# Optimization experiments

Hardware: AMD Instinct MI355X
Metric: run time of the kernel (lower is better)

The kernel has to match this reference:

```python
import jax, jax.numpy as jnp
import numpy as np

N_NODES = 100000
N_EDGES = 1600000
N_GRAPHS = 128
H = 64          # hidden_channels_gin
L = 3           # num_layers
IN_X = 4
IN_E = 8
G_DIM = H * L   # pooled concat dim = hidden_channels_global
OUT = 1


def _w(k, shape):
    return (jax.random.normal(k, shape, jnp.float32) * 0.1)


def setup_inputs() -> dict:
    key = jax.random.key(0)
    ks = jax.random.split(key, 24)
    inp = {
        'x': jax.random.normal(ks[0], (N_NODES, IN_X), jnp.float32),
        'edge_index': jax.random.randint(ks[1], (2, N_EDGES), 0, N_NODES),
        'batch': jnp.sort(jax.random.randint(ks[2], (N_NODES,), 0, N_GRAPHS)),
        'edge_attr': jax.random.normal(ks[3], (N_EDGES, IN_E), jnp.float32),
        # node embedding MLP (MLPembd: Linear-ReLU-Linear-ReLU-Linear)
        'nW1': _w(ks[4], (IN_X, H)), 'nb1': jnp.zeros((H,), jnp.float32),
        'nW2': _w(ks[5], (H, H)),    'nb2': jnp.zeros((H,), jnp.float32),
        'nW3': _w(ks[6], (H, H)),    'nb3': jnp.zeros((H,), jnp.float32),
        # edge embedding MLP (gin_MLP_layers[0])
        'eW1': _w(ks[7], (IN_E, H)), 'eb1': jnp.zeros((H,), jnp.float32),
        'eW2': _w(ks[8], (H, H)),    'eb2': jnp.zeros((H,), jnp.float32),
        'eW3': _w(ks[9], (H, H)),    'eb3': jnp.zeros((H,), jnp.float32),
        # GINE layers: trainable eps + 2-layer MLP nn per layer (stacked over L)
        'gine_eps': jnp.zeros((L,), jnp.float32),
        'gW1': _w(ks[10], (L, H, H)), 'gb1': jnp.zeros((L, H), jnp.float32),
        'gW2': _w(ks[11], (L, H, H)), 'gb2': jnp.zeros((L, H), jnp.float32),
        # output MLP: Linear - BN(eval) - LeakyReLU - (Dropout eval) - Linear
        'oW1': _w(ks[12], (G_DIM, G_DIM)), 'ob1': jnp.zeros((G_DIM,), jnp.float32),
        'ogamma': jnp.ones((G_DIM,), jnp.float32), 'obeta': jnp.zeros((G_DIM,), jnp.float32),
        'oW2': _w(ks[13], (G_DIM, OUT)), 'ob2': jnp.zeros((OUT,), jnp.float32),
    }
    return inp


def _mlp3(x, W1, b1, W2, b2, W3, b3):
    x = jax.nn.relu(x @ W1 + b1)
    x = jax.nn.relu(x @ W2 + b2)
    return x @ W3 + b3


def _forward(x, edge_index, batch, edge_attr,
             nW1, nb1, nW2, nb2, nW3, nb3,
             eW1, eb1, eW2, eb2, eW3, eb3,
             gine_eps, gW1, gb1, gW2, gb2,
             oW1, ob1, ogamma, obeta, oW2, ob2):
    src, dst = edge_index[0], edge_index[1]
    h = _mlp3(x, nW1, nb1, nW2, nb2, nW3, nb3)                    # [N, H]
    ea = _mlp3(edge_attr, eW1, eb1, eW2, eb2, eW3, eb3)           # [E, H]
    pooled = []
    for l in range(L):  # fixed small layer count
        msg = jax.nn.leaky_relu(h[src] + ea)                      # [E, H] gather + add
        agg = jax.ops.segment_max(msg, dst, num_segments=N_NODES) # max aggregation
        agg = jnp.where(jnp.isfinite(agg), agg, 0.0)              # isolated nodes -> 0
        z = (1.0 + gine_eps[l]) * h + agg
        h = jax.nn.leaky_relu(z @ gW1[l] + gb1[l]) @ gW2[l] + gb2[l]
        pooled.append(jax.ops.segment_max(h, batch, num_segments=N_GRAPHS))
    hp = jnp.concatenate(pooled, axis=1)                          # [G, H*L]
    y = hp @ oW1 + ob1
    y = ogamma * y + obeta            # eval-mode BatchNorm1d (running mean=0, var=1)
    y = jax.nn.leaky_relu(y)          # Dropout inactive at inference
    logits = y @ oW2 + ob2            # [G, 1]
    return logits, jax.nn.sigmoid(logits)


def reference(x, edge_index, batch, edge_attr,
              nW1, nb1, nW2, nb2, nW3, nb3,
              eW1, eb1, eW2, eb2, eW3, eb3,
              gine_eps, gW1, gb1, gW2, gb2,
              oW1, ob1, ogamma, obeta, oW2, ob2):
    return _forward(x, edge_index, batch, edge_attr,
                    nW1, nb1, nW2, nb2, nW3, nb3,
                    eW1, eb1, eW2, eb2, eW3, eb3,
                    gine_eps, gW1, gb1, gW2, gb2,
                    oW1, ob1, ogamma, obeta, oW2, ob2)
```

## Files before the change

kernel.cpp:

```cpp
#include <hip/hip_runtime.h>
#include <hip/hip_bf16.h>

#define LRELU(x) ((x) > 0.0f ? (x) : 0.01f * (x))

typedef __attribute__((ext_vector_type(4))) short bf16x4;
typedef __attribute__((ext_vector_type(4))) float f32x4;

__device__ __forceinline__ unsigned fenc(float f) {
    unsigned u = __float_as_uint(f);
    return (u & 0x80000000u) ? ~u : (u | 0x80000000u);
}
__device__ __forceinline__ float fdec(unsigned u) {
    return (u & 0x80000000u) ? __uint_as_float(u & 0x7fffffffu) : __uint_as_float(~u);
}
__device__ __forceinline__ short f2bf(float f) {
    __hip_bfloat16 b = __float2bfloat16(f);
    return *reinterpret_cast<short*>(&b);
}
__device__ __forceinline__ float bf2f(short s) {
    return __uint_as_float(((unsigned)(unsigned short)s) << 16);
}

__device__ __forceinline__ f32x4 mfma16(bf16x4 a, bf16x4 b, f32x4 c) {
#if __has_builtin(__builtin_amdgcn_mfma_f32_16x16x16bf16_1k)
    return __builtin_amdgcn_mfma_f32_16x16x16bf16_1k(a, b, c, 0, 0, 0);
#else
    asm("v_mfma_f32_16x16x16_bf16 %0, %1, %2, %0" : "+v"(c) : "v"(a), "v"(b));
    return c;
#endif
}

__global__ __launch_bounds__(256) void hist_kernel(const int* __restrict__ ei,
                                                   int* __restrict__ deg_p,
                                                   int* __restrict__ rank, int E)
{
    const int stride = gridDim.x * blockDim.x * 4;
    const bool vec = ((E & 3) == 0);
    for (int e4 = (blockIdx.x * blockDim.x + threadIdx.x) * 4; e4 < E; e4 += stride) {
        if (vec && e4 + 3 < E) {
            const int4 d = *reinterpret_cast<const int4*>(ei + E + e4);
            int4 r;
            r.x = atomicAdd(&deg_p[(size_t)d.x * 4], 1);
            r.y = atomicAdd(&deg_p[(size_t)d.y * 4], 1);
            r.z = atomicAdd(&deg_p[(size_t)d.z * 4], 1);
            r.w = atomicAdd(&deg_p[(size_t)d.w * 4], 1);
            *reinterpret_cast<int4*>(rank + e4) = r;
        } else {
            for (int k = 0; k < 4 && e4 + k < E; ++k) {
                const int d = ei[E + e4 + k];
                rank[e4 + k] = atomicAdd(&deg_p[(size_t)d * 4], 1);
            }
        }
    }
}

__global__ __launch_bounds__(1024) void scan_kernel(const int* __restrict__ deg_p,
                                                    int* __restrict__ rowptr, int N)
{
    __shared__ int wsum[16];
    __shared__ int tiletot;
    const int lane = threadIdx.x & 63;
    const int w    = threadIdx.x >> 6;
    int carry = 0;
    for (int base = 0; base < N; base += 4096) {
        const int i = base + (int)threadIdx.x * 4;
        int4 v = {0, 0, 0, 0};
        if (i < N)     v.x = deg_p[(size_t)i * 4];
        if (i + 1 < N) v.y = deg_p[(size_t)(i + 1) * 4];
        if (i + 2 < N) v.z = deg_p[(size_t)(i + 2) * 4];
        if (i + 3 < N) v.w = deg_p[(size_t)(i + 3) * 4];
        const int tot = v.x + v.y + v.z + v.w;
        int s = tot;
#pragma unroll
        for (int off = 1; off < 64; off <<= 1) {
            int t = __shfl_up(s, off);
            if (lane >= off) s += t;
        }
        if (lane == 63) wsum[w] = s;
        __syncthreads();
        if (threadIdx.x == 0) {
            int acc = 0;
#pragma unroll
            for (int k = 0; k < 16; ++k) { int t = wsum[k]; wsum[k] = acc; acc += t; }
            tiletot = acc;
        }
        __syncthreads();
        const int excl = carry + wsum[w] + (s - tot);
        int4 o;
        o.x = excl; o.y = excl + v.x; o.z = o.y + v.y; o.w = o.z + v.z;
        if (i + 3 < N) {
            *reinterpret_cast<int4*>(rowptr + i) = o;
        } else {
            if (i < N)     rowptr[i] = o.x;
            if (i + 1 < N) rowptr[i + 1] = o.y;
            if (i + 2 < N) rowptr[i + 2] = o.z;
        }
        carry += tiletot;
        __syncthreads();
    }
    if (threadIdx.x == 0) rowptr[N] = carry;
}

__global__ __launch_bounds__(256) void scatter_kernel(
    const int* __restrict__ ei, const int* __restrict__ rank,
    const int* __restrict__ rowptr, int2* __restrict__ pack, int E)
{
    const int stride = gridDim.x * blockDim.x * 4;
    const bool vec = ((E & 3) == 0);
    for (int e4 = (blockIdx.x * blockDim.x + threadIdx.x) * 4; e4 < E; e4 += stride) {
        if (vec && e4 + 3 < E) {
            const int4 s  = *reinterpret_cast<const int4*>(ei + e4);
            const int4 d  = *reinterpret_cast<const int4*>(ei + E + e4);
            const int4 rk = *reinterpret_cast<const int4*>(rank + e4);
            pack[rowptr[d.x] + rk.x] = make_int2(s.x, e4 + 0);
            pack[rowptr[d.y] + rk.y] = make_int2(s.y, e4 + 1);
            pack[rowptr[d.z] + rk.z] = make_int2(s.z, e4 + 2);
            pack[rowptr[d.w] + rk.w] = make_int2(s.w, e4 + 3);
        } else {
            for (int k = 0; k < 4 && e4 + k < E; ++k) {
                const int e = e4 + k;
                pack[rowptr[ei[E + e]] + rank[e]] = make_int2(ei[e], e);
            }
        }
    }
}

__global__ __launch_bounds__(256) void edge_mlp_mfma(
    const float* __restrict__ eattr, const int2* __restrict__ pack,
    const float* __restrict__ W1, const float* __restrict__ b1,
    const float* __restrict__ W2, const float* __restrict__ b2,
    const float* __restrict__ W3, const float* __restrict__ b3,
    short* __restrict__ eout, int E)
{
    const int lane = threadIdx.x & 63;
    const int el   = lane & 15;
    const int g    = lane >> 4;

    bf16x4 w1f[4];
    bf16x4 w2f[4][4];
    bf16x4 w3f[4][4];
    f32x4  bf1[4], bf2[4], bf3[4];
#pragma unroll
    for (int t = 0; t < 4; ++t) {
        const int c = t * 16 + el;
#pragma unroll
        for (int j = 0; j < 4; ++j) {
            const int k = g * 4 + j;
            w1f[t][j] = (k < 8) ? f2bf(W1[k * 64 + c]) : (short)0;
        }
#pragma unroll
        for (int kb = 0; kb < 4; ++kb) {
#pragma unroll
            for (int j = 0; j < 4; ++j) {
                const int k = kb * 16 + g * 4 + j;
                w2f[t][kb][j] = f2bf(W2[k * 64 + c]);
                w3f[t][kb][j] = f2bf(W3[k * 64 + c]);
            }
        }
        const float4 v1 = *reinterpret_cast<const float4*>(b1 + t * 16 + g * 4);
        const float4 v2 = *reinterpret_cast<const float4*>(b2 + t * 16 + g * 4);
        const float4 v3 = *reinterpret_cast<const float4*>(b3 + t * 16 + g * 4);
        bf1[t][0] = v1.x; bf1[t][1] = v1.y; bf1[t][2] = v1.z; bf1[t][3] = v1.w;
        bf2[t][0] = v2.x; bf2[t][1] = v2.y; bf2[t][2] = v2.z; bf2[t][3] = v2.w;
        bf3[t][0] = v3.x; bf3[t][1] = v3.y; bf3[t][2] = v3.z; bf3[t][3] = v3.w;
    }

    const int nblk = (E + 15) >> 4;
    const int wid  = (int)((blockIdx.x * blockDim.x + threadIdx.x) >> 6);
    const int nw   = (int)((gridDim.x * blockDim.x) >> 6);

    for (int eb = wid; eb < nblk; eb += nw) {
        const int e  = eb * 16 + el;
        const int ec = min(e, E - 1);
        const int eid = pack[ec].y;

        bf16x4 bfr = (bf16x4)0;
        if (g < 2) {
            const float4 av = *reinterpret_cast<const float4*>(eattr + (size_t)eid * 8 + g * 4);
            bfr[0] = f2bf(av.x); bfr[1] = f2bf(av.y);
            bfr[2] = f2bf(av.z); bfr[3] = f2bf(av.w);
        }

        f32x4  acc[4];
        bf16x4 act[4];

#pragma unroll
        for (int t = 0; t < 4; ++t) acc[t] = mfma16(w1f[t], bfr, bf1[t]);
#pragma unroll
        for (int t = 0; t < 4; ++t)
#pragma unroll
            for (int j = 0; j < 4; ++j) act[t][j] = f2bf(fmaxf(acc[t][j], 0.0f));

#pragma unroll
        for (int t = 0; t < 4; ++t) {
            f32x4 a = bf2[t];
#pragma unroll
            for (int kb = 0; kb < 4; ++kb) a = mfma16(w2f[t][kb], act[kb], a);
            acc[t] = a;
        }
#pragma unroll
        for (int t = 0; t < 4; ++t)
#pragma unroll
            for (int j = 0; j < 4; ++j) act[t][j] = f2bf(fmaxf(acc[t][j], 0.0f));

#pragma unroll
        for (int t = 0; t < 4; ++t) {
            f32x4 a = bf3[t];
#pragma unroll
            for (int kb = 0; kb < 4; ++kb) a = mfma16(w3f[t][kb], act[kb], a);
            bf16x4 o;
#pragma unroll
            for (int j = 0; j < 4; ++j) o[j] = f2bf(a[j]);
            if (e < E)
                *reinterpret_cast<bf16x4*>(eout + (size_t)e * 64 + t * 16 + g * 4) = o;
        }
    }
}

__global__ __launch_bounds__(256) void node_mlp_mfma(
    const float* __restrict__ x,
    const float* __restrict__ W1, const float* __restrict__ b1,
    const float* __restrict__ W2, const float* __restrict__ b2,
    const float* __restrict__ W3, const float* __restrict__ b3,
    short* __restrict__ hout, int N)
{
    const int lane = threadIdx.x & 63;
    const int el   = lane & 15;
    const int g    = lane >> 4;

    bf16x4 w1f[4];
    bf16x4 w2f[4][4];
    bf16x4 w3f[4][4];
    f32x4  bf1[4], bf2[4], bf3[4];
#pragma unroll
    for (int t = 0; t < 4; ++t) {
        const int c = t * 16 + el;
#pragma unroll
        for (int j = 0; j < 4; ++j) {
            const int k = g * 4 + j;
            w1f[t][j] = (k < 4) ? f2bf(W1[k * 64 + c]) : (short)0;
        }
#pragma unroll
        for (int kb = 0; kb < 4; ++kb) {
#pragma unroll
            for (int j = 0; j < 4; ++j) {
                const int k = kb * 16 + g * 4 + j;
                w2f[t][kb][j] = f2bf(W2[k * 64 + c]);
                w3f[t][kb][j] = f2bf(W3[k * 64 + c]);
            }
        }
        const float4 v1 = *reinterpret_cast<const float4*>(b1 + t * 16 + g * 4);
        const float4 v2 = *reinterpret_cast<const float4*>(b2 + t * 16 + g * 4);
        const float4 v3 = *reinterpret_cast<const float4*>(b3 + t * 16 + g * 4);
        bf1[t][0] = v1.x; bf1[t][1] = v1.y; bf1[t][2] = v1.z; bf1[t][3] = v1.w;
        bf2[t][0] = v2.x; bf2[t][1] = v2.y; bf2[t][2] = v2.z; bf2[t][3] = v2.w;
        bf3[t][0] = v3.x; bf3[t][1] = v3.y; bf3[t][2] = v3.z; bf3[t][3] = v3.w;
    }

    const int nblk = (N + 15) >> 4;
    const int wid  = (int)((blockIdx.x * blockDim.x + threadIdx.x) >> 6);
    const int nw   = (int)((gridDim.x * blockDim.x) >> 6);

    for (int nb = wid; nb < nblk; nb += nw) {
        const int n  = nb * 16 + el;
        const int nc = min(n, N - 1);

        bf16x4 bfr = (bf16x4)0;
        if (g == 0) {
            const float4 xv = *reinterpret_cast<const float4*>(x + (size_t)nc * 4);
            bfr[0] = f2bf(xv.x); bfr[1] = f2bf(xv.y);
            bfr[2] = f2bf(xv.z); bfr[3] = f2bf(xv.w);
        }

        f32x4  acc[4];
        bf16x4 act[4];
#pragma unroll
        for (int t = 0; t < 4; ++t) acc[t] = mfma16(w1f[t], bfr, bf1[t]);
#pragma unroll
        for (int t = 0; t < 4; ++t)
#pragma unroll
            for (int j = 0; j < 4; ++j) act[t][j] = f2bf(fmaxf(acc[t][j], 0.0f));

#pragma unroll
        for (int t = 0; t < 4; ++t) {
            f32x4 a = bf2[t];
#pragma unroll
            for (int kb = 0; kb < 4; ++kb) a = mfma16(w2f[t][kb], act[kb], a);
            acc[t] = a;
        }
#pragma unroll
        for (int t = 0; t < 4; ++t)
#pragma unroll
            for (int j = 0; j < 4; ++j) act[t][j] = f2bf(fmaxf(acc[t][j], 0.0f));

#pragma unroll
        for (int t = 0; t < 4; ++t) {
            f32x4 a = bf3[t];
#pragma unroll
            for (int kb = 0; kb < 4; ++kb) a = mfma16(w3f[t][kb], act[kb], a);
            bf16x4 o;
#pragma unroll
            for (int j = 0; j < 4; ++j) o[j] = f2bf(a[j]);
            if (n < N)
                *reinterpret_cast<bf16x4*>(hout + (size_t)n * 64 + t * 16 + g * 4) = o;
        }
    }
}

__global__ __launch_bounds__(256) void agg_kernel(
    const short* __restrict__ h_in, short* __restrict__ z_out,
    const int* __restrict__ rowptr, const int2* __restrict__ pack,
    const short* __restrict__ ea,
    const float* __restrict__ geps, int l, int N)
{
    const int lane = threadIdx.x & 63;
    const int g    = lane >> 4;
    const int el   = lane & 15;
    const float ope = 1.0f + geps[l];

    const int nwave = gridDim.x * 4;
    const int w     = blockIdx.x * 4 + (threadIdx.x >> 6);
    const int chunk = (N + nwave - 1) / nwave;
    const int n0 = w * chunk;
    const int n1 = min(N, n0 + chunk);
    if (n0 >= n1) return;

    int r0 = rowptr[n0];
    for (int n = n0; n < n1; ++n) {
        const int r1 = rowptr[n + 1];

        float m0 = -INFINITY, m1 = -INFINITY, m2 = -INFINITY, m3 = -INFINITY;
        for (int r = r0; r < r1; r += 16) {
#pragma unroll
            for (int u = 0; u < 4; ++u) {
                const int rc = min(r + u * 4 + g, r1 - 1);
                const int s  = pack[rc].x;
                const bf16x4 hv = *reinterpret_cast<const bf16x4*>(h_in + (size_t)s * 64 + el * 4);
                const bf16x4 ev = *reinterpret_cast<const bf16x4*>(ea + (size_t)rc * 64 + el * 4);
                float c0 = bf2f(hv[0]) + bf2f(ev[0]);
                float c1 = bf2f(hv[1]) + bf2f(ev[1]);
                float c2 = bf2f(hv[2]) + bf2f(ev[2]);
                float c3 = bf2f(hv[3]) + bf2f(ev[3]);
                c0 = LRELU(c0); c1 = LRELU(c1); c2 = LRELU(c2); c3 = LRELU(c3);
                m0 = fmaxf(m0, c0); m1 = fmaxf(m1, c1);
                m2 = fmaxf(m2, c2); m3 = fmaxf(m3, c3);
            }
        }
        m0 = fmaxf(m0, __shfl_xor(m0, 16)); m0 = fmaxf(m0, __shfl_xor(m0, 32));
        m1 = fmaxf(m1, __shfl_xor(m1, 16)); m1 = fmaxf(m1, __shfl_xor(m1, 32));
        m2 = fmaxf(m2, __shfl_xor(m2, 16)); m2 = fmaxf(m2, __shfl_xor(m2, 32));
        m3 = fmaxf(m3, __shfl_xor(m3, 16)); m3 = fmaxf(m3, __shfl_xor(m3, 32));

        if (g == 0) {
            const bf16x4 hn = *reinterpret_cast<const bf16x4*>(h_in + (size_t)n * 64 + el * 4);
            bf16x4 zo;
            zo[0] = f2bf(ope * bf2f(hn[0]) + ((m0 == -INFINITY) ? 0.0f : m0));
            zo[1] = f2bf(ope * bf2f(hn[1]) + ((m1 == -INFINITY) ? 0.0f : m1));
            zo[2] = f2bf(ope * bf2f(hn[2]) + ((m2 == -INFINITY) ? 0.0f : m2));
            zo[3] = f2bf(ope * bf2f(hn[3]) + ((m3 == -INFINITY) ? 0.0f : m3));
            *reinterpret_cast<bf16x4*>(z_out + (size_t)n * 64 + el * 4) = zo;
        }
        r0 = r1;
    }
}

__global__ __launch_bounds__(256) void mlp_pool_kernel(
    const short* __restrict__ z, short* __restrict__ h_out,
    const int* __restrict__ batch,
    const float* __restrict__ gW1, const float* __restrict__ gb1,
    const float* __restrict__ gW2, const float* __restrict__ gb2,
    unsigned* __restrict__ pooled, int l, int N)
{
    const int lane = threadIdx.x & 63;
    const int el   = lane & 15;
    const int g    = lane >> 4;

    const float* W1 = gW1 + (size_t)l * 4096;
    const float* W2 = gW2 + (size_t)l * 4096;
    bf16x4 w1f[4][4], w2f[4][4];
    f32x4  bA[4], bB[4];
#pragma unroll
    for (int t = 0; t < 4; ++t) {
        const int c = t * 16 + el;
#pragma unroll
        for (int kb = 0; kb < 4; ++kb) {
#pragma unroll
            for (int j = 0; j < 4; ++j) {
                const int k = kb * 16 + g * 4 + j;
                w1f[t][kb][j] = f2bf(W1[k * 64 + c]);
                w2f[t][kb][j] = f2bf(W2[k * 64 + c]);
            }
        }
        const float4 v1 = *reinterpret_cast<const float4*>(gb1 + l * 64 + t * 16 + g * 4);
        const float4 v2 = *reinterpret_cast<const float4*>(gb2 + l * 64 + t * 16 + g * 4);
        bA[t][0] = v1.x; bA[t][1] = v1.y; bA[t][2] = v1.z; bA[t][3] = v1.w;
        bB[t][0] = v2.x; bB[t][1] = v2.y; bB[t][2] = v2.z; bB[t][3] = v2.w;
    }

    const int nblk = (N + 15) >> 4;
    const int wid  = (int)((blockIdx.x * blockDim.x + threadIdx.x) >> 6);
    const int nw   = (int)((gridDim.x * blockDim.x) >> 6);

    for (int nb = wid; nb < nblk; nb += nw) {
        const int n  = nb * 16 + el;
        const bool valid = (n < N);
        const int nc = valid ? n : (N - 1);

        bf16x4 zf[4];
#pragma unroll
        for (int kb = 0; kb < 4; ++kb)
            zf[kb] = *reinterpret_cast<const bf16x4*>(z + (size_t)nc * 64 + kb * 16 + g * 4);

        f32x4  acc[4];
        bf16x4 act[4];
#pragma unroll
        for (int t = 0; t < 4; ++t) {
            f32x4 a = bA[t];
#pragma unroll
            for (int kb = 0; kb < 4; ++kb) a = mfma16(w1f[t][kb], zf[kb], a);
            acc[t] = a;
        }
#pragma unroll
        for (int t = 0; t < 4; ++t)
#pragma unroll
            for (int j = 0; j < 4; ++j) act[t][j] = f2bf(LRELU(acc[t][j]));

#pragma unroll
        for (int t = 0; t < 4; ++t) {
            f32x4 a = bB[t];
#pragma unroll
            for (int kb = 0; kb < 4; ++kb) a = mfma16(w2f[t][kb], act[kb], a);
            acc[t] = a;
        }

#pragma unroll
        for (int t = 0; t < 4; ++t) {
            bf16x4 o;
#pragma unroll
            for (int j = 0; j < 4; ++j) o[j] = f2bf(acc[t][j]);
            if (valid)
                *reinterpret_cast<bf16x4*>(h_out + (size_t)n * 64 + t * 16 + g * 4) = o;
        }

        const int gbl = batch[nc];
        const int gb_first = __shfl(gbl, 0);
        const int gb_last  = __shfl(gbl, 15);
        if (gb_first == gb_last) {
#pragma unroll
            for (int t = 0; t < 4; ++t) {
#pragma unroll
                for (int j = 0; j < 4; ++j) {
                    float v = valid ? acc[t][j] : -INFINITY;
                    v = fmaxf(v, __shfl_xor(v, 1));
                    v = fmaxf(v, __shfl_xor(v, 2));
                    v = fmaxf(v, __shfl_xor(v, 4));
                    v = fmaxf(v, __shfl_xor(v, 8));
                    if (el == 0)
                        atomicMax(&pooled[gb_first * 192 + l * 64 + t * 16 + g * 4 + j], fenc(v));
                }
            }
        } else if (valid) {
#pragma unroll
            for (int t = 0; t < 4; ++t)
#pragma unroll
                for (int j = 0; j < 4; ++j)
                    atomicMax(&pooled[gbl * 192 + l * 64 + t * 16 + g * 4 + j], fenc(acc[t][j]));
        }
    }
}

__global__ __launch_bounds__(192) void out_kernel(
    const unsigned* __restrict__ pooled,
    const float* __restrict__ oW1, const float* __restrict__ ob1,
    const float* __restrict__ ogamma, const float* __restrict__ obeta,
    const float* __restrict__ oW2, const float* __restrict__ ob2,
    float* __restrict__ out)
{
    __shared__ float hp[192];
    __shared__ float partial[3];
    const int c = threadIdx.x;
    const int g = blockIdx.x;

    const unsigned u = pooled[g * 192 + c];
    hp[c] = (u == 0u) ? -INFINITY : fdec(u);
    __syncthreads();

    float y = ob1[c];
#pragma unroll 4
    for (int k = 0; k < 192; ++k)
        y += hp[k] * oW1[k * 192 + c];
    y = ogamma[c] * y + obeta[c];
    y = LRELU(y);
    float contrib = y * oW2[c];

#pragma unroll
    for (int off = 32; off > 0; off >>= 1)
        contrib += __shfl_xor(contrib, off);
    if ((threadIdx.x & 63) == 0) partial[threadIdx.x >> 6] = contrib;
    __syncthreads();
    if (threadIdx.x == 0) {
        const float logit = partial[0] + partial[1] + partial[2] + ob2[0];
        out[g] = logit;
        out[128 + g] = 1.0f / (1.0f + expf(-logit));
    }
}

extern "C" void kernel_launch(void* const* d_in, const int* in_sizes, int n_in,
                              void* d_out, int out_size, void* d_ws, size_t ws_size,
                              hipStream_t stream)
{
    const float* x     = (const float*)d_in[0];
    const int*   ei    = (const int*)d_in[1];
    const int*   batch = (const int*)d_in[2];
    const float* eattr = (const float*)d_in[3];
    const float* nW1 = (const float*)d_in[4],  *nb1 = (const float*)d_in[5];
    const float* nW2 = (const float*)d_in[6],  *nb2 = (const float*)d_in[7];
    const float* nW3 = (const float*)d_in[8],  *nb3 = (const float*)d_in[9];
    const float* eW1 = (const float*)d_in[10], *eb1 = (const float*)d_in[11];
    const float* eW2 = (const float*)d_in[12], *eb2 = (const float*)d_in[13];
    const float* eW3 = (const float*)d_in[14], *eb3 = (const float*)d_in[15];
    const float* geps = (const float*)d_in[16];
    const float* gW1 = (const float*)d_in[17], *gb1 = (const float*)d_in[18];
    const float* gW2 = (const float*)d_in[19], *gb2 = (const float*)d_in[20];
    const float* oW1 = (const float*)d_in[21], *ob1 = (const float*)d_in[22];
    const float* ogamma = (const float*)d_in[23], *obeta = (const float*)d_in[24];
    const float* oW2 = (const float*)d_in[25], *ob2 = (const float*)d_in[26];
    float* out = (float*)d_out;

    const int N = in_sizes[0] / 4;
    const int E = in_sizes[3] / 8;
    const size_t EP = ((size_t)E + 15) & ~(size_t)15;

    char* ws = (char*)d_ws;
    size_t off = 0;
    auto take = [&](size_t bytes) { char* p = ws + off; off += (bytes + 255) & ~(size_t)255; return p; };
    short*    ea     = (short*)take(EP * 64 * sizeof(short));
    short*    h0     = (short*)take((size_t)N * 64 * sizeof(short));
    short*    h1     = (short*)take((size_t)N * 64 * sizeof(short));
    int2*     pack   = (int2*)take((size_t)E * sizeof(int2));
    short*    zbuf   = (short*)take((size_t)N * 64 * sizeof(short));
    int*      rank   = (int*)take((size_t)E * sizeof(int));
    int*      rowptr = (int*)take(((size_t)N + 1) * sizeof(int));
    unsigned* pooled = (unsigned*)take(128 * 192 * sizeof(unsigned));
    int* deg_p = (int*)h1;
    (void)ws_size;

    hipMemsetAsync(pooled, 0, 128 * 192 * sizeof(unsigned), stream);
    hipMemsetAsync(deg_p, 0, (size_t)N * 4 * sizeof(int), stream);

    const int gEdge = (E / 4 + 255) / 256 + 1;
    hist_kernel<<<gEdge, 256, 0, stream>>>(ei, deg_p, rank, E);
    scan_kernel<<<1, 1024, 0, stream>>>(deg_p, rowptr, N);
    node_mlp_mfma<<<1024, 256, 0, stream>>>(x, nW1, nb1, nW2, nb2, nW3, nb3, h0, N);
    scatter_kernel<<<gEdge, 256, 0, stream>>>(ei, rank, rowptr, pack, E);
    edge_mlp_mfma<<<2048, 256, 0, stream>>>(eattr, pack, eW1, eb1, eW2, eb2, eW3, eb3, ea, E);

    for (int l = 0; l < 3; ++l) {
        const short* hi = (l & 1) ? h1 : h0;
        short*       ho = (l & 1) ? h0 : h1;
        agg_kernel<<<2048, 256, 0, stream>>>(hi, zbuf, rowptr, pack, ea, geps, l, N);
        mlp_pool_kernel<<<1024, 256, 0, stream>>>(zbuf, ho, batch,
                                                  gW1, gb1, gW2, gb2, pooled, l, N);
    }

    out_kernel<<<128, 192, 0, stream>>>(pooled, oW1, ob1, ogamma, obeta, oW2, ob2, out);
}
```

Before: 713.9 us.

## Recompute edge MLP inside aggregation kernel instead of materializing edge embeddings

Removes the separate edge-MLP kernel and its E x 64 bf16 edge-embedding buffer. The aggregation kernel now reruns the 3-layer edge MLP with MFMA for each 16-edge chunk, once per GINE layer, reading only the 8-float edge attributes. The first-layer bias is folded into the MFMA through a constant-one input column. This trades roughly 200MB of edge-embedding writes and reads for three times the edge-MLP compute, plus extra register pressure and cross-lane shuffle reductions in the aggregation kernel.

Result: slower. 1.089 ms (+52.6%).

```diff
diff --git a/kernel.cpp b/kernel.cpp
--- a/kernel.cpp
+++ b/kernel.cpp
@@ -125,12 +125,12 @@
     }
 }
 
-__global__ __launch_bounds__(256) void edge_mlp_mfma(
-    const float* __restrict__ eattr, const int2* __restrict__ pack,
+__global__ __launch_bounds__(256) void node_mlp_mfma(
+    const float* __restrict__ x,
     const float* __restrict__ W1, const float* __restrict__ b1,
     const float* __restrict__ W2, const float* __restrict__ b2,
     const float* __restrict__ W3, const float* __restrict__ b3,
-    short* __restrict__ eout, int E)
+    short* __restrict__ hout, int N)
 {
     const int lane = threadIdx.x & 63;
     const int el   = lane & 15;
@@ -146,7 +146,7 @@
 #pragma unroll
         for (int j = 0; j < 4; ++j) {
             const int k = g * 4 + j;
-            w1f[t][j] = (k < 8) ? f2bf(W1[k * 64 + c]) : (short)0;
+            w1f[t][j] = (k < 4) ? f2bf(W1[k * 64 + c]) : (short)0;
         }
 #pragma unroll
         for (int kb = 0; kb < 4; ++kb) {
@@ -165,98 +165,6 @@
         bf3[t][0] = v3.x; bf3[t][1] = v3.y; bf3[t][2] = v3.z; bf3[t][3] = v3.w;
     }
 
-    const int nblk = (E + 15) >> 4;
-    const int wid  = (int)((blockIdx.x * blockDim.x + threadIdx.x) >> 6);
-    const int nw   = (int)((gridDim.x * blockDim.x) >> 6);
-
-    for (int eb = wid; eb < nblk; eb += nw) {
-        const int e  = eb * 16 + el;
-        const int ec = min(e, E - 1);
-        const int eid = pack[ec].y;
-
-        bf16x4 bfr = (bf16x4)0;
-        if (g < 2) {
-            const float4 av = *reinterpret_cast<const float4*>(eattr + (size_t)eid * 8 + g * 4);
-            bfr[0] = f2bf(av.x); bfr[1] = f2bf(av.y);
-            bfr[2] = f2bf(av.z); bfr[3] = f2bf(av.w);
-        }
-
-        f32x4  acc[4];
-        bf16x4 act[4];
-
-#pragma unroll
-        for (int t = 0; t < 4; ++t) acc[t] = mfma16(w1f[t], bfr, bf1[t]);
-#pragma unroll
-        for (int t = 0; t < 4; ++t)
-#pragma unroll
-            for (int j = 0; j < 4; ++j) act[t][j] = f2bf(fmaxf(acc[t][j], 0.0f));
-
-#pragma unroll
-        for (int t = 0; t < 4; ++t) {
-            f32x4 a = bf2[t];
-#pragma unroll
-            for (int kb = 0; kb < 4; ++kb) a = mfma16(w2f[t][kb], act[kb], a);
-            acc[t] = a;
-        }
-#pragma unroll
-        for (int t = 0; t < 4; ++t)
-#pragma unroll
-            for (int j = 0; j < 4; ++j) act[t][j] = f2bf(fmaxf(acc[t][j], 0.0f));
-
-#pragma unroll
-        for (int t = 0; t < 4; ++t) {
-            f32x4 a = bf3[t];
-#pragma unroll
-            for (int kb = 0; kb < 4; ++kb) a = mfma16(w3f[t][kb], act[kb], a);
-            bf16x4 o;
-#pragma unroll
-            for (int j = 0; j < 4; ++j) o[j] = f2bf(a[j]);
-            if (e < E)
-                *reinterpret_cast<bf16x4*>(eout + (size_t)e * 64 + t * 16 + g * 4) = o;
-        }
-    }
-}
-
-__global__ __launch_bounds__(256) void node_mlp_mfma(
-    const float* __restrict__ x,
-    const float* __restrict__ W1, const float* __restrict__ b1,
-    const float* __restrict__ W2, const float* __restrict__ b2,
-    const float* __restrict__ W3, const float* __restrict__ b3,
-    short* __restrict__ hout, int N)
-{
-    const int lane = threadIdx.x & 63;
-    const int el   = lane & 15;
-    const int g    = lane >> 4;
-
-    bf16x4 w1f[4];
-    bf16x4 w2f[4][4];
-    bf16x4 w3f[4][4];
-    f32x4  bf1[4], bf2[4], bf3[4];
-#pragma unroll
-    for (int t = 0; t < 4; ++t) {
-        const int c = t * 16 + el;
-#pragma unroll
-        for (int j = 0; j < 4; ++j) {
-            const int k = g * 4 + j;
-            w1f[t][j] = (k < 4) ? f2bf(W1[k * 64 + c]) : (short)0;
-        }
-#pragma unroll
-        for (int kb = 0; kb < 4; ++kb) {
-#pragma unroll
-            for (int j = 0; j < 4; ++j) {
-                const int k = kb * 16 + g * 4 + j;
-                w2f[t][kb][j] = f2bf(W2[k * 64 + c]);
-                w3f[t][kb][j] = f2bf(W3[k * 64 + c]);
-            }
-        }
-        const float4 v1 = *reinterpret_cast<const float4*>(b1 + t * 16 + g * 4);
-        const float4 v2 = *reinterpret_cast<const float4*>(b2 + t * 16 + g * 4);
-        const float4 v3 = *reinterpret_cast<const float4*>(b3 + t * 16 + g * 4);
-        bf1[t][0] = v1.x; bf1[t][1] = v1.y; bf1[t][2] = v1.z; bf1[t][3] = v1.w;
-        bf2[t][0] = v2.x; bf2[t][1] = v2.y; bf2[t][2] = v2.z; bf2[t][3] = v2.w;
-        bf3[t][0] = v3.x; bf3[t][1] = v3.y; bf3[t][2] = v3.z; bf3[t][3] = v3.w;
-    }
-
     const int nblk = (N + 15) >> 4;
     const int wid  = (int)((blockIdx.x * blockDim.x + threadIdx.x) >> 6);
     const int nw   = (int)((gridDim.x * blockDim.x) >> 6);
@@ -307,16 +215,47 @@
     }
 }
 
-__global__ __launch_bounds__(256) void agg_kernel(
+__global__ __launch_bounds__(256) void agg_mlp_fused(
     const short* __restrict__ h_in, short* __restrict__ z_out,
     const int* __restrict__ rowptr, const int2* __restrict__ pack,
-    const short* __restrict__ ea,
+    const float* __restrict__ eattr,
+    const float* __restrict__ W1, const float* __restrict__ b1,
+    const float* __restrict__ W2, const float* __restrict__ b2,
+    const float* __restrict__ W3, const float* __restrict__ b3,
     const float* __restrict__ geps, int l, int N)
 {
     const int lane = threadIdx.x & 63;
+    const int el   = lane & 15;
     const int g    = lane >> 4;
-    const int el   = lane & 15;
     const float ope = 1.0f + geps[l];
+
+    bf16x4 w1f[4];
+    bf16x4 w2f[4][4];
+    bf16x4 w3f[4][4];
+    f32x4  bf2_[4], bf3_[4];
+#pragma unroll
+    for (int t = 0; t < 4; ++t) {
+        const int c = t * 16 + el;
+#pragma unroll
+        for (int j = 0; j < 4; ++j) {
+            const int k = g * 4 + j;
+            w1f[t][j] = (k < 8) ? f2bf(W1[k * 64 + c])
+                       : ((k == 8) ? f2bf(b1[c]) : (short)0);
+        }
+#pragma unroll
+        for (int kb = 0; kb < 4; ++kb) {
+#pragma unroll
+            for (int j = 0; j < 4; ++j) {
+                const int k = kb * 16 + g * 4 + j;
+                w2f[t][kb][j] = f2bf(W2[k * 64 + c]);
+                w3f[t][kb][j] = f2bf(W3[k * 64 + c]);
+            }
+        }
+        const float4 v2 = *reinterpret_cast<const float4*>(b2 + t * 16 + g * 4);
+        const float4 v3 = *reinterpret_cast<const float4*>(b3 + t * 16 + g * 4);
+        bf2_[t][0] = v2.x; bf2_[t][1] = v2.y; bf2_[t][2] = v2.z; bf2_[t][3] = v2.w;
+        bf3_[t][0] = v3.x; bf3_[t][1] = v3.y; bf3_[t][2] = v3.z; bf3_[t][3] = v3.w;
+    }
 
     const int nwave = gridDim.x * 4;
     const int w     = blockIdx.x * 4 + (threadIdx.x >> 6);
@@ -329,36 +268,89 @@
     for (int n = n0; n < n1; ++n) {
         const int r1 = rowptr[n + 1];
 
-        float m0 = -INFINITY, m1 = -INFINITY, m2 = -INFINITY, m3 = -INFINITY;
-        for (int r = r0; r < r1; r += 16) {
-#pragma unroll
-            for (int u = 0; u < 4; ++u) {
-                const int rc = min(r + u * 4 + g, r1 - 1);
-                const int s  = pack[rc].x;
-                const bf16x4 hv = *reinterpret_cast<const bf16x4*>(h_in + (size_t)s * 64 + el * 4);
-                const bf16x4 ev = *reinterpret_cast<const bf16x4*>(ea + (size_t)rc * 64 + el * 4);
-                float c0 = bf2f(hv[0]) + bf2f(ev[0]);
-                float c1 = bf2f(hv[1]) + bf2f(ev[1]);
-                float c2 = bf2f(hv[2]) + bf2f(ev[2]);
-                float c3 = bf2f(hv[3]) + bf2f(ev[3]);
-                c0 = LRELU(c0); c1 = LRELU(c1); c2 = LRELU(c2); c3 = LRELU(c3);
-                m0 = fmaxf(m0, c0); m1 = fmaxf(m1, c1);
-                m2 = fmaxf(m2, c2); m3 = fmaxf(m3, c3);
-            }
-        }
-        m0 = fmaxf(m0, __shfl_xor(m0, 16)); m0 = fmaxf(m0, __shfl_xor(m0, 32));
-        m1 = fmaxf(m1, __shfl_xor(m1, 16)); m1 = fmaxf(m1, __shfl_xor(m1, 32));
-        m2 = fmaxf(m2, __shfl_xor(m2, 16)); m2 = fmaxf(m2, __shfl_xor(m2, 32));
-        m3 = fmaxf(m3, __shfl_xor(m3, 16)); m3 = fmaxf(m3, __shfl_xor(m3, 32));
-
-        if (g == 0) {
-            const bf16x4 hn = *reinterpret_cast<const bf16x4*>(h_in + (size_t)n * 64 + el * 4);
-            bf16x4 zo;
-            zo[0] = f2bf(ope * bf2f(hn[0]) + ((m0 == -INFINITY) ? 0.0f : m0));
-            zo[1] = f2bf(ope * bf2f(hn[1]) + ((m1 == -INFINITY) ? 0.0f : m1));
-            zo[2] = f2bf(ope * bf2f(hn[2]) + ((m2 == -INFINITY) ? 0.0f : m2));
-            zo[3] = f2bf(ope * bf2f(hn[3]) + ((m3 == -INFINITY) ? 0.0f : m3));
-            *reinterpret_cast<bf16x4*>(z_out + (size_t)n * 64 + el * 4) = zo;
+        f32x4 m4[4];
+#pragma unroll
+        for (int t = 0; t < 4; ++t)
+#pragma unroll
+            for (int j = 0; j < 4; ++j) m4[t][j] = -INFINITY;
+
+        for (int rb = r0; rb < r1; rb += 16) {
+            const int2 pk = pack[min(rb + el, r1 - 1)];
+
+            bf16x4 bfr = (bf16x4)0;
+            if (g < 2) {
+                const float4 av = *reinterpret_cast<const float4*>(
+                    eattr + (size_t)pk.y * 8 + g * 4);
+                bfr[0] = f2bf(av.x); bfr[1] = f2bf(av.y);
+                bfr[2] = f2bf(av.z); bfr[3] = f2bf(av.w);
+            } else if (g == 2) {
+                bfr[0] = (short)0x3F80;
+            }
+
+            f32x4  acc[4];
+            bf16x4 act[4];
+            const f32x4 z4 = {0.f, 0.f, 0.f, 0.f};
+#pragma unroll
+            for (int t = 0; t < 4; ++t) acc[t] = mfma16(w1f[t], bfr, z4);
+#pragma unroll
+            for (int t = 0; t < 4; ++t)
+#pragma unroll
+                for (int j = 0; j < 4; ++j) act[t][j] = f2bf(fmaxf(acc[t][j], 0.0f));
+
+#pragma unroll
+            for (int t = 0; t < 4; ++t) {
+                f32x4 a = bf2_[t];
+#pragma unroll
+                for (int kb = 0; kb < 4; ++kb) a = mfma16(w2f[t][kb], act[kb], a);
+                acc[t] = a;
+            }
+#pragma unroll
+            for (int t = 0; t < 4; ++t)
+#pragma unroll
+                for (int j = 0; j < 4; ++j) act[t][j] = f2bf(fmaxf(acc[t][j], 0.0f));
+
+#pragma unroll
+            for (int t = 0; t < 4; ++t) {
+                f32x4 a = bf3_[t];
+#pragma unroll
+                for (int kb = 0; kb < 4; ++kb) a = mfma16(w3f[t][kb], act[kb], a);
+                const bf16x4 hv = *reinterpret_cast<const bf16x4*>(
+                    h_in + (size_t)pk.x * 64 + t * 16 + g * 4);
+#pragma unroll
+                for (int j = 0; j < 4; ++j) {
+                    float cv = bf2f(hv[j]) + a[j];
+                    cv = LRELU(cv);
+                    m4[t][j] = fmaxf(m4[t][j], cv);
+                }
+            }
+        }
+
+#pragma unroll
+        for (int t = 0; t < 4; ++t) {
+#pragma unroll
+            for (int j = 0; j < 4; ++j) {
+                float v = m4[t][j];
+                v = fmaxf(v, __shfl_xor(v, 1));
+                v = fmaxf(v, __shfl_xor(v, 2));
+                v = fmaxf(v, __shfl_xor(v, 4));
+                v = fmaxf(v, __shfl_xor(v, 8));
+                m4[t][j] = v;
+            }
+        }
+
+        if (el == 0) {
+#pragma unroll
+            for (int t = 0; t < 4; ++t) {
+                const bf16x4 hn = *reinterpret_cast<const bf16x4*>(
+                    h_in + (size_t)n * 64 + t * 16 + g * 4);
+                bf16x4 zo;
+#pragma unroll
+                for (int j = 0; j < 4; ++j) {
+                    const float mv = (m4[t][j] == -INFINITY) ? 0.0f : m4[t][j];
+                    zo[j] = f2bf(ope * bf2f(hn[j]) + mv);
+                }
+                *reinterpret_cast<bf16x4*>(z_out + (size_t)n * 64 + t * 16 + g * 4) = zo;
+            }
         }
         r0 = r1;
     }
@@ -529,12 +521,10 @@
 
     const int N = in_sizes[0] / 4;
     const int E = in_sizes[3] / 8;
-    const size_t EP = ((size_t)E + 15) & ~(size_t)15;
 
     char* ws = (char*)d_ws;
     size_t off = 0;
     auto take = [&](size_t bytes) { char* p = ws + off; off += (bytes + 255) & ~(size_t)255; return p; };
-    short*    ea     = (short*)take(EP * 64 * sizeof(short));
     short*    h0     = (short*)take((size_t)N * 64 * sizeof(short));
     short*    h1     = (short*)take((size_t)N * 64 * sizeof(short));
     int2*     pack   = (int2*)take((size_t)E * sizeof(int2));
@@ -553,12 +543,13 @@
     scan_kernel<<<1, 1024, 0, stream>>>(deg_p, rowptr, N);
     node_mlp_mfma<<<1024, 256, 0, stream>>>(x, nW1, nb1, nW2, nb2, nW3, nb3, h0, N);
     scatter_kernel<<<gEdge, 256, 0, stream>>>(ei, rank, rowptr, pack, E);
-    edge_mlp_mfma<<<2048, 256, 0, stream>>>(eattr, pack, eW1, eb1, eW2, eb2, eW3, eb3, ea, E);
 
     for (int l = 0; l < 3; ++l) {
         const short* hi = (l & 1) ? h1 : h0;
         short*       ho = (l & 1) ? h0 : h1;
-        agg_kernel<<<2048, 256, 0, stream>>>(hi, zbuf, rowptr, pack, ea, geps, l, N);
+        agg_mlp_fused<<<2048, 256, 0, stream>>>(hi, zbuf, rowptr, pack, eattr,
+                                                eW1, eb1, eW2, eb2, eW3, eb3,
+                                                geps, l, N);
         mlp_pool_kernel<<<1024, 256, 0, stream>>>(zbuf, ho, batch,
                                                   gW1, gb1, gW2, gb2, pooled, l, N);
     }
```
